# Performance work log

Measured on AMD Instinct MI355X. Metric: run time of the kernel, lower is better.

Reference implementation:

```python
import jax, jax.numpy as jnp
import numpy as np

HEADS = 8


def setup_inputs() -> dict:
    key = jax.random.key(0)
    k1, k2, k3, k4, k5, k6 = jax.random.split(key, 6)
    B, S, E = 2, 2048, 512
    D = E // HEADS
    return {
        "values": jax.random.normal(k1, (B, S, E), dtype=jnp.float32),
        "keys": jax.random.normal(k2, (B, S, E), dtype=jnp.float32),
        "queries": jax.random.normal(k3, (B, S, E), dtype=jnp.float32),
        "mask": jax.random.randint(k4, (B, 1, 1, S), 0, 2, dtype=jnp.int32),
        "W_v": jax.random.normal(k5, (D, D), dtype=jnp.float32) * (1.0 / np.sqrt(D)),
        "W_o": jax.random.normal(k6, (E, E), dtype=jnp.float32) * (1.0 / np.sqrt(E)),
        "b_o": jnp.zeros((E,), dtype=jnp.float32),
    }


def reference(values, keys, queries, mask, W_v, W_o, b_o):
    B, S, E = queries.shape
    H = HEADS
    D = E // H
    # reshape to (b, s, h, d) and apply the SAME W_v linear to v, k, q
    # (faithful to the original, which calls self.values on all three)
    v = jnp.einsum('bshd,ed->bshe', values.reshape(B, -1, H, D), W_v)
    k = jnp.einsum('bshd,ed->bshe', keys.reshape(B, -1, H, D), W_v)
    q = jnp.einsum('bshd,ed->bshe', queries.reshape(B, -1, H, D), W_v)
    # unscaled attention scores (original has no 1/sqrt(d))
    energy = jnp.einsum('bqhd,bkhd->bhqk', q, k)  # (b, h, q, k)
    energy = jnp.where(mask == 0, -jnp.inf, energy)
    attn = jax.nn.softmax(energy, axis=3)
    out = jnp.einsum('bhqk,bkhd->bqhd', attn, v)  # (b, q, h, d)
    out = out.reshape(B, S, E)
    return out @ W_o.T + b_o
```

## Files before the change

kernel.cpp:

```cpp
#include <hip/hip_runtime.h>


#define B_ 2
#define S_ 2048
#define E_ 512
#define H_ 8
#define D_ 64

#define LOG2E 1.4426950408889634f
#define KEEP_BIAS (-92.332483f)

typedef unsigned short ushort_t;
typedef __attribute__((ext_vector_type(8))) short short8;
typedef __attribute__((ext_vector_type(8))) _Float16 half8;
typedef __attribute__((ext_vector_type(4))) float f32x4;

__device__ __forceinline__ ushort_t f2bs(float x) {
    union { float f; unsigned int u; } a; a.f = x;
    unsigned int u = a.u;
    u += 0x7fffu + ((u >> 16) & 1u);
    return (ushort_t)(u >> 16);
}
__device__ __forceinline__ float bs2f(ushort_t h) {
    union { unsigned int u; float f; } a; a.u = ((unsigned int)h) << 16;
    return a.f;
}
__device__ __forceinline__ ushort_t f2hs(float x) {
    _Float16 h = (_Float16)x;
    ushort_t u; __builtin_memcpy(&u, &h, 2);
    return u;
}
__device__ __forceinline__ void split16(const float4* g, ushort_t* hi, ushort_t* lo) {
    #pragma unroll
    for (int q = 0; q < 4; ++q) {
        float4 f = g[q];
        float vv[4] = {f.x, f.y, f.z, f.w};
        #pragma unroll
        for (int j = 0; j < 4; ++j) {
            ushort_t h = f2bs(vv[j]);
            hi[q * 4 + j] = h;
            lo[q * 4 + j] = f2bs(vv[j] - bs2f(h));
        }
    }
}

__global__ void __launch_bounds__(256) proj_mfma(
    const float* __restrict__ quer, const float* __restrict__ keys,
    const float* __restrict__ vals, const float* __restrict__ Wv,
    const float* __restrict__ Wo,
    ushort_t* __restrict__ qf, ushort_t* __restrict__ kf,
    ushort_t* __restrict__ vt, ushort_t* __restrict__ Wob)
{
    __shared__ ushort_t Ah[64 * 72], Al[64 * 72];
    __shared__ ushort_t Bh[64 * 72], Bl[64 * 72];
    const int tens = blockIdx.y;
    const int bx = blockIdx.x;
    const int t = threadIdx.x;

    if (tens == 3) {
        if (bx < 128) {
            int g = (bx * 256 + t) * 8;
            float4 f0 = *(const float4*)(Wo + g);
            float4 f1 = *(const float4*)(Wo + g + 4);
            ushort_t tmp[8] = {f2bs(f0.x), f2bs(f0.y), f2bs(f0.z), f2bs(f0.w),
                               f2bs(f1.x), f2bs(f1.y), f2bs(f1.z), f2bs(f1.w)};
            *(uint4*)&Wob[g] = *(uint4*)tmp;
        }
        return;
    }

    const float* src = tens == 0 ? quer : (tens == 1 ? keys : vals);
    const int st = bx & 31, bh = bx >> 5;
    const int b = bh >> 3, h = bh & 7;
    const int s0 = st * 64;

    {
        int e = t >> 2, dg = (t & 3) * 16;
        ushort_t th[16], tl[16];
        split16((const float4*)(Wv + e * 64 + dg), th, tl);
        *(uint4*)&Bh[e * 72 + dg] = *(uint4*)th;  *(uint4*)&Bh[e * 72 + dg + 8] = *(uint4*)(th + 8);
        *(uint4*)&Bl[e * 72 + dg] = *(uint4*)tl;  *(uint4*)&Bl[e * 72 + dg + 8] = *(uint4*)(tl + 8);
    }
    {
        int row = t >> 2, cg = (t & 3) * 16;
        const float* g = src + ((size_t)b * S_ + s0 + row) * 512 + h * 64 + cg;
        ushort_t th[16], tl[16];
        split16((const float4*)g, th, tl);
        *(uint4*)&Ah[row * 72 + cg] = *(uint4*)th;  *(uint4*)&Ah[row * 72 + cg + 8] = *(uint4*)(th + 8);
        *(uint4*)&Al[row * 72 + cg] = *(uint4*)tl;  *(uint4*)&Al[row * 72 + cg + 8] = *(uint4*)(tl + 8);
    }
    __syncthreads();

    const int w = t >> 6, lm = t & 15, quad = (t >> 4) & 3;
    f32x4 acc[4];
    #pragma unroll
    for (int nt = 0; nt < 4; ++nt) acc[nt] = (f32x4){0.f, 0.f, 0.f, 0.f};

    __builtin_amdgcn_s_setprio(1);
    #pragma unroll
    for (int kk = 0; kk < 2; ++kk) {
        short8 ah = *(const short8*)&Ah[(w * 16 + lm) * 72 + kk * 32 + quad * 8];
        short8 al = *(const short8*)&Al[(w * 16 + lm) * 72 + kk * 32 + quad * 8];
        #pragma unroll
        for (int nt = 0; nt < 4; ++nt) {
            short8 bh8 = *(const short8*)&Bh[(nt * 16 + lm) * 72 + kk * 32 + quad * 8];
            short8 bl8 = *(const short8*)&Bl[(nt * 16 + lm) * 72 + kk * 32 + quad * 8];
            acc[nt] = __builtin_amdgcn_mfma_f32_16x16x32_bf16(ah, bh8, acc[nt], 0, 0, 0);
            acc[nt] = __builtin_amdgcn_mfma_f32_16x16x32_bf16(al, bh8, acc[nt], 0, 0, 0);
            acc[nt] = __builtin_amdgcn_mfma_f32_16x16x32_bf16(ah, bl8, acc[nt], 0, 0, 0);
        }
    }
    __builtin_amdgcn_s_setprio(0);

    if (tens < 2) {
        ushort_t* dst = tens == 0 ? qf : kf;
        const float sc = tens == 0 ? LOG2E : 1.0f;
        #pragma unroll
        for (int nt = 0; nt < 4; ++nt) {
            #pragma unroll
            for (int r = 0; r < 4; ++r) {
                size_t addr = ((size_t)bh * S_ + s0 + w * 16 + quad * 4 + r) * 64 + nt * 16 + lm;
                dst[addr] = f2hs(acc[nt][r] * sc);
            }
        }
    } else {
        #pragma unroll
        for (int nt = 0; nt < 4; ++nt) {
            unsigned int p0 = (unsigned int)f2bs(acc[nt][0]) | ((unsigned int)f2bs(acc[nt][1]) << 16);
            unsigned int p1 = (unsigned int)f2bs(acc[nt][2]) | ((unsigned int)f2bs(acc[nt][3]) << 16);
            uint2 pk; pk.x = p0; pk.y = p1;
            size_t addr = ((size_t)bh * 64 + nt * 16 + lm) * S_ + s0 + w * 16 + quad * 4;
            *(uint2*)&vt[addr] = pk;
        }
    }
}

__global__ void __launch_bounds__(512, 4) attn_mfma(
    const ushort_t* __restrict__ qf, const ushort_t* __restrict__ kf,
    const ushort_t* __restrict__ vt, const int* __restrict__ mask,
    ushort_t* __restrict__ ctx)
{
    __shared__ ushort_t Ks[2][64 * 72];
    __shared__ ushort_t Vt[2][64 * 72];
    __shared__ ushort_t Ps[8 * 16 * 72];
    __shared__ float    mb[2][64];

    const int bx = blockIdx.x;
    const int qt = bx & 31;
    const int bh = bx >> 5;
    const int b  = bh >> 3;
    const int t  = threadIdx.x;
    const int w  = t >> 6;
    const int wq = w & 3;
    const int ws = w >> 2;
    const int lm = t & 15, quad = (t >> 4) & 3;
    const int q0 = qt * 64;
    const int wbase = w * 16 * 72;

    const int srow = t >> 3;
    const int scg  = (t & 7) * 8;
    const size_t kgbase = ((size_t)bh * S_ + srow) * 64 + scg;
    const size_t vgbase = ((size_t)bh * 64 + srow) * S_ + scg;

    half8 aq[2];
    {
        size_t qrow = ((size_t)bh * S_ + q0 + wq * 16 + lm) * 64 + quad * 8;
        aq[0] = *(const half8*)&qf[qrow];
        aq[1] = *(const half8*)&qf[qrow + 32];
    }
    short8 ones;
    #pragma unroll
    for (int j = 0; j < 8; ++j) ones[j] = (short)0x3F80;

    f32x4 acc[4];
    #pragma unroll
    for (int nt = 0; nt < 4; ++nt) acc[nt] = (f32x4){0.f, 0.f, 0.f, 0.f};
    f32x4 acc_l = (f32x4){0.f, 0.f, 0.f, 0.f};

    {
        *(uint4*)&Ks[0][srow * 72 + scg] = *(const uint4*)&kf[kgbase];
        *(uint4*)&Ks[1][srow * 72 + scg] = *(const uint4*)&kf[kgbase + 4096];
        *(uint4*)&Vt[0][srow * 72 + scg] = *(const uint4*)&vt[vgbase];
        *(uint4*)&Vt[1][srow * 72 + scg] = *(const uint4*)&vt[vgbase + 64];
        if (t < 128) mb[t >> 6][t & 63] = mask[b * S_ + t] ? KEEP_BIAS : -1e30f;
    }
    __syncthreads();

    for (int is = 0; is < S_ / 128; ++is) {
        const bool pf = (is + 1) < (S_ / 128);

        uint4 pk0, pk1, pv0, pv1; int mnx = 0;
        if (pf) {
            size_t ko = kgbase + (size_t)(2 * (is + 1)) * 4096;
            pk0 = *(const uint4*)&kf[ko];
            pk1 = *(const uint4*)&kf[ko + 4096];
            size_t vo = vgbase + (size_t)(2 * (is + 1)) * 64;
            pv0 = *(const uint4*)&vt[vo];
            pv1 = *(const uint4*)&vt[vo + 64];
            if (t < 128) mnx = mask[b * S_ + (2 * (is + 1)) * 64 + t];
        }

        const ushort_t* Kc = Ks[ws];
        const ushort_t* Vc = Vt[ws];

        #pragma unroll
        for (int nt = 0; nt < 4; ++nt) {
            f32x4 s = *(const f32x4*)&mb[ws][nt * 16 + quad * 4];
            __builtin_amdgcn_s_setprio(1);
            #pragma unroll
            for (int kk = 0; kk < 2; ++kk) {
                half8 ak = *(const half8*)&Kc[(nt * 16 + lm) * 72 + kk * 32 + quad * 8];
                s = __builtin_amdgcn_mfma_f32_16x16x32_f16(ak, aq[kk], s, 0, 0, 0);
            }
            __builtin_amdgcn_s_setprio(0);
            float p0 = __builtin_amdgcn_exp2f(s[0]);
            float p1 = __builtin_amdgcn_exp2f(s[1]);
            float p2 = __builtin_amdgcn_exp2f(s[2]);
            float p3 = __builtin_amdgcn_exp2f(s[3]);
            uint2 pkd;
            pkd.x = (unsigned int)f2bs(p0) | ((unsigned int)f2bs(p1) << 16);
            pkd.y = (unsigned int)f2bs(p2) | ((unsigned int)f2bs(p3) << 16);
            *(uint2*)&Ps[wbase + lm * 72 + nt * 16 + quad * 4] = pkd;
        }

        __builtin_amdgcn_s_setprio(1);
        #pragma unroll
        for (int kk = 0; kk < 2; ++kk) {
            short8 ap = *(const short8*)&Ps[wbase + lm * 72 + kk * 32 + quad * 8];
            #pragma unroll
            for (int nt = 0; nt < 4; ++nt) {
                short8 bv = *(const short8*)&Vc[(nt * 16 + lm) * 72 + kk * 32 + quad * 8];
                acc[nt] = __builtin_amdgcn_mfma_f32_16x16x32_bf16(ap, bv, acc[nt], 0, 0, 0);
            }
            acc_l = __builtin_amdgcn_mfma_f32_16x16x32_bf16(ap, ones, acc_l, 0, 0, 0);
        }
        __builtin_amdgcn_s_setprio(0);

        __syncthreads();
        if (pf) {
            *(uint4*)&Ks[0][srow * 72 + scg] = pk0;
            *(uint4*)&Ks[1][srow * 72 + scg] = pk1;
            *(uint4*)&Vt[0][srow * 72 + scg] = pv0;
            *(uint4*)&Vt[1][srow * 72 + scg] = pv1;
            if (t < 128) mb[t >> 6][t & 63] = mnx ? KEEP_BIAS : -1e30f;
            __syncthreads();
        }
    }

    float* cf = (float*)Ps;
    const int lane = t & 63;
    __syncthreads();
    if (ws == 1) {
        const int base = (wq * 64 + lane) * 18;
        #pragma unroll
        for (int nt = 0; nt < 4; ++nt) {
            #pragma unroll
            for (int r = 0; r < 4; r += 2) {
                float2 v2; v2.x = acc[nt][r]; v2.y = acc[nt][r + 1];
                *(float2*)&cf[base + nt * 4 + r] = v2;
            }
        }
    }
    __syncthreads();
    if (ws == 0) {
        const int base = (wq * 64 + lane) * 18;
        #pragma unroll
        for (int nt = 0; nt < 4; ++nt) {
            #pragma unroll
            for (int r = 0; r < 4; ++r) acc[nt][r] += cf[base + nt * 4 + r];
        }
    }
    __syncthreads();
    if (ws == 1) {
        const int base = (wq * 64 + lane) * 5;
        #pragma unroll
        for (int r = 0; r < 4; ++r) cf[base + r] = acc_l[r];
    }
    __syncthreads();

    if (ws == 0) {
        const int base = (wq * 64 + lane) * 5;
        #pragma unroll
        for (int r = 0; r < 4; ++r) acc_l[r] += cf[base + r];
        const int h = bh & 7;
        #pragma unroll
        for (int r = 0; r < 4; ++r) {
            float inv = 1.f / acc_l[r];
            int s = q0 + wq * 16 + quad * 4 + r;
            #pragma unroll
            for (int nt = 0; nt < 4; ++nt) {
                int d = nt * 16 + lm;
                ctx[((size_t)b * S_ + s) * E_ + h * D_ + d] = f2bs(acc[nt][r] * inv);
            }
        }
    }
}

__global__ void __launch_bounds__(512, 4) outproj_mfma(
    const ushort_t* __restrict__ ctx, const ushort_t* __restrict__ Wob,
    const float* __restrict__ bo, float* __restrict__ out)
{
    __shared__ ushort_t sm[4][64 * 72];
    const int m0 = blockIdx.x * 64, n0 = blockIdx.y * 64;
    const int t = threadIdx.x;
    const int w = t >> 6, wq = w & 3, wk = w >> 2;
    const int lm = t & 15, quad = (t >> 4) & 3;
    const int srow = t >> 3, scg = (t & 7) * 8;

    const size_t abase = (size_t)(m0 + srow) * E_ + scg;
    const size_t bbase = (size_t)(n0 + srow) * E_ + scg;

    f32x4 acc[4];
    #pragma unroll
    for (int nt = 0; nt < 4; ++nt) acc[nt] = (f32x4){0.f, 0.f, 0.f, 0.f};

    *(uint4*)&sm[0][srow * 72 + scg] = *(const uint4*)&ctx[abase];
    *(uint4*)&sm[1][srow * 72 + scg] = *(const uint4*)&ctx[abase + 256];
    *(uint4*)&sm[2][srow * 72 + scg] = *(const uint4*)&Wob[bbase];
    *(uint4*)&sm[3][srow * 72 + scg] = *(const uint4*)&Wob[bbase + 256];
    __syncthreads();

    const ushort_t* Ac = sm[wk];
    const ushort_t* Bc = sm[2 + wk];

    for (int is = 0; is < 4; ++is) {
        const bool pf = is < 3;
        uint4 pa0, pa1, pb0, pb1;
        if (pf) {
            pa0 = *(const uint4*)&ctx[abase + (size_t)(is + 1) * 64];
            pa1 = *(const uint4*)&ctx[abase + 256 + (size_t)(is + 1) * 64];
            pb0 = *(const uint4*)&Wob[bbase + (size_t)(is + 1) * 64];
            pb1 = *(const uint4*)&Wob[bbase + 256 + (size_t)(is + 1) * 64];
        }

        __builtin_amdgcn_s_setprio(1);
        #pragma unroll
        for (int kk = 0; kk < 2; ++kk) {
            short8 a = *(const short8*)&Ac[(wq * 16 + lm) * 72 + kk * 32 + quad * 8];
            #pragma unroll
            for (int nt = 0; nt < 4; ++nt) {
                short8 bb = *(const short8*)&Bc[(nt * 16 + lm) * 72 + kk * 32 + quad * 8];
                acc[nt] = __builtin_amdgcn_mfma_f32_16x16x32_bf16(a, bb, acc[nt], 0, 0, 0);
            }
        }
        __builtin_amdgcn_s_setprio(0);

        __syncthreads();
        if (pf) {
            *(uint4*)&sm[0][srow * 72 + scg] = pa0;
            *(uint4*)&sm[1][srow * 72 + scg] = pa1;
            *(uint4*)&sm[2][srow * 72 + scg] = pb0;
            *(uint4*)&sm[3][srow * 72 + scg] = pb1;
            __syncthreads();
        }
    }

    float* cf = (float*)sm;
    const int lane = t & 63;
    if (wk == 1) {
        const int base = (wq * 64 + lane) * 18;
        #pragma unroll
        for (int nt = 0; nt < 4; ++nt) {
            #pragma unroll
            for (int r = 0; r < 4; r += 2) {
                float2 v2; v2.x = acc[nt][r]; v2.y = acc[nt][r + 1];
                *(float2*)&cf[base + nt * 4 + r] = v2;
            }
        }
    }
    __syncthreads();
    if (wk == 0) {
        const int base = (wq * 64 + lane) * 18;
        #pragma unroll
        for (int nt = 0; nt < 4; ++nt) {
            float bias = bo[n0 + nt * 16 + lm];
            #pragma unroll
            for (int r = 0; r < 4; ++r) {
                int m = m0 + wq * 16 + quad * 4 + r;
                out[(size_t)m * E_ + n0 + nt * 16 + lm] =
                    acc[nt][r] + cf[base + nt * 4 + r] + bias;
            }
        }
    }
}

extern "C" void kernel_launch(void* const* d_in, const int* in_sizes, int n_in,
                              void* d_out, int out_size, void* d_ws, size_t ws_size,
                              hipStream_t stream) {
    const float* vals = (const float*)d_in[0];
    const float* keys = (const float*)d_in[1];
    const float* quer = (const float*)d_in[2];
    const int*   mask = (const int*)d_in[3];
    const float* Wv   = (const float*)d_in[4];
    const float* Wo   = (const float*)d_in[5];
    const float* bo   = (const float*)d_in[6];
    float* out = (float*)d_out;

    const size_t N = (size_t)B_ * H_ * S_ * D_;
    ushort_t* ws  = (ushort_t*)d_ws;
    ushort_t* qf  = ws;
    ushort_t* kf  = ws + N;
    ushort_t* vt  = ws + 2 * N;
    ushort_t* ctx = ws + 3 * N;
    ushort_t* Wob = ws + 4 * N;

    proj_mfma<<<dim3(B_ * H_ * (S_ / 64), 4), 256, 0, stream>>>(
        quer, keys, vals, Wv, Wo, qf, kf, vt, Wob);
    attn_mfma<<<B_ * H_ * (S_ / 64), 512, 0, stream>>>(qf, kf, vt, mask, ctx);
    outproj_mfma<<<dim3((B_ * S_) / 64, E_ / 64), 512, 0, stream>>>(ctx, Wob, bo, out);
}
```

Baseline: 131.4 us.

## Give each attention wave 32 queries and split keys four ways

Each wave now covers 32 query rows, sharing every loaded K fragment and V fragment across two query groups. Waves are laid out as 2 query groups by 4 key splits with 256-key stages, and each wave stages a whole 64-row K or V tile. The combine becomes a two-level tree reduction through shared memory, and block indices are swizzled to spread heads across CUs. The aim is fewer LDS reads per MFMA and fewer barriers, at the cost of more registers and LDS, reflected in launch bounds lowered to 2 blocks per CU.

```diff
diff --git a/kernel.cpp b/kernel.cpp
--- a/kernel.cpp
+++ b/kernel.cpp
@@ -135,69 +135,77 @@
     }
 }
 
-__global__ void __launch_bounds__(512, 4) attn_mfma(
+__global__ void __launch_bounds__(512, 2) attn_mfma(
     const ushort_t* __restrict__ qf, const ushort_t* __restrict__ kf,
     const ushort_t* __restrict__ vt, const int* __restrict__ mask,
     ushort_t* __restrict__ ctx)
 {
-    __shared__ ushort_t Ks[2][64 * 72];
-    __shared__ ushort_t Vt[2][64 * 72];
-    __shared__ ushort_t Ps[8 * 16 * 72];
-    __shared__ float    mb[2][64];
-
-    const int bx = blockIdx.x;
+    __shared__ ushort_t Ks[4][64 * 72];
+    __shared__ ushort_t Vt[4][64 * 72];
+    __shared__ ushort_t Ps[8][32 * 72];
+    __shared__ float    mb[4][64];
+
+    const int bx0 = blockIdx.x;
+    const int bx = (bx0 & 7) * 64 + (bx0 >> 3);
     const int qt = bx & 31;
     const int bh = bx >> 5;
     const int b  = bh >> 3;
     const int t  = threadIdx.x;
     const int w  = t >> 6;
-    const int wq = w & 3;
-    const int ws = w >> 2;
+    const int wq = w & 1;
+    const int ws = w >> 1;
     const int lm = t & 15, quad = (t >> 4) & 3;
+    const int lane = t & 63;
     const int q0 = qt * 64;
-    const int wbase = w * 16 * 72;
-
-    const int srow = t >> 3;
-    const int scg  = (t & 7) * 8;
-    const size_t kgbase = ((size_t)bh * S_ + srow) * 64 + scg;
-    const size_t vgbase = ((size_t)bh * 64 + srow) * S_ + scg;
-
-    half8 aq[2];
+
+    const int stile = w & 3;
+    const bool isV = w >= 4;
+    const size_t kstage0 = ((size_t)bh * S_ + stile * 64 + lane) * 64;
+    const size_t vstage0 = ((size_t)bh * 64 + lane) * S_ + stile * 64;
+    ushort_t* sdst = isV ? &Vt[stile][lane * 72] : &Ks[stile][lane * 72];
+    const ushort_t* sgl = isV ? vt : kf;
+    const size_t sg0 = isV ? vstage0 : kstage0;
+    const size_t sgstep = isV ? 256 : 16384;
+
+    half8 aq[2][2];
+    #pragma unroll
+    for (int qg = 0; qg < 2; ++qg) {
+        size_t qrow = ((size_t)bh * S_ + q0 + wq * 32 + qg * 16 + lm) * 64 + quad * 8;
+        aq[qg][0] = *(const half8*)&qf[qrow];
+        aq[qg][1] = *(const half8*)&qf[qrow + 32];
+    }
+    short8 ones;
+    #pragma unroll
+    for (int j = 0; j < 8; ++j) ones[j] = (short)0x3F80;
+
+    f32x4 acc[2][4];
+    f32x4 accl[2];
+    #pragma unroll
+    for (int qg = 0; qg < 2; ++qg) {
+        accl[qg] = (f32x4){0.f, 0.f, 0.f, 0.f};
+        #pragma unroll
+        for (int nt = 0; nt < 4; ++nt) acc[qg][nt] = (f32x4){0.f, 0.f, 0.f, 0.f};
+    }
+
     {
-        size_t qrow = ((size_t)bh * S_ + q0 + wq * 16 + lm) * 64 + quad * 8;
-        aq[0] = *(const half8*)&qf[qrow];
-        aq[1] = *(const half8*)&qf[qrow + 32];
-    }
-    short8 ones;
-    #pragma unroll
-    for (int j = 0; j < 8; ++j) ones[j] = (short)0x3F80;
-
-    f32x4 acc[4];
-    #pragma unroll
-    for (int nt = 0; nt < 4; ++nt) acc[nt] = (f32x4){0.f, 0.f, 0.f, 0.f};
-    f32x4 acc_l = (f32x4){0.f, 0.f, 0.f, 0.f};
-
-    {
-        *(uint4*)&Ks[0][srow * 72 + scg] = *(const uint4*)&kf[kgbase];
-        *(uint4*)&Ks[1][srow * 72 + scg] = *(const uint4*)&kf[kgbase + 4096];
-        *(uint4*)&Vt[0][srow * 72 + scg] = *(const uint4*)&vt[vgbase];
-        *(uint4*)&Vt[1][srow * 72 + scg] = *(const uint4*)&vt[vgbase + 64];
-        if (t < 128) mb[t >> 6][t & 63] = mask[b * S_ + t] ? KEEP_BIAS : -1e30f;
-    }
-    __syncthreads();
-
-    for (int is = 0; is < S_ / 128; ++is) {
-        const bool pf = (is + 1) < (S_ / 128);
-
-        uint4 pk0, pk1, pv0, pv1; int mnx = 0;
+        uint4 st[8];
+        #pragma unroll
+        for (int j = 0; j < 8; ++j) st[j] = *(const uint4*)&sgl[sg0 + j * 8];
+        #pragma unroll
+        for (int j = 0; j < 8; ++j) *(uint4*)&sdst[j * 8] = st[j];
+        if (t < 256) mb[t >> 6][t & 63] = mask[b * S_ + t] ? KEEP_BIAS : -1e30f;
+    }
+    __syncthreads();
+
+    for (int is = 0; is < 8; ++is) {
+        const bool pf = is < 7;
+
+        uint4 st[8]; int mnx = 0;
         if (pf) {
-            size_t ko = kgbase + (size_t)(2 * (is + 1)) * 4096;
-            pk0 = *(const uint4*)&kf[ko];
-            pk1 = *(const uint4*)&kf[ko + 4096];
-            size_t vo = vgbase + (size_t)(2 * (is + 1)) * 64;
-            pv0 = *(const uint4*)&vt[vo];
-            pv1 = *(const uint4*)&vt[vo + 64];
-            if (t < 128) mnx = mask[b * S_ + (2 * (is + 1)) * 64 + t];
+            size_t g = sg0 + (size_t)(is + 1) * sgstep;
+            #pragma unroll
+            for (int j = 0; j < 8; ++j) st[j] = *(const uint4*)&sgl[g + j * 8];
+            if (t < 256) mnx = mask[b * S_ + (is + 1) * 256 + t];
         }
 
         const ushort_t* Kc = Ks[ws];
@@ -205,92 +213,117 @@
 
         #pragma unroll
         for (int nt = 0; nt < 4; ++nt) {
-            f32x4 s = *(const f32x4*)&mb[ws][nt * 16 + quad * 4];
+            f32x4 binit = *(const f32x4*)&mb[ws][nt * 16 + quad * 4];
+            f32x4 s0v = binit, s1v = binit;
             __builtin_amdgcn_s_setprio(1);
             #pragma unroll
             for (int kk = 0; kk < 2; ++kk) {
                 half8 ak = *(const half8*)&Kc[(nt * 16 + lm) * 72 + kk * 32 + quad * 8];
-                s = __builtin_amdgcn_mfma_f32_16x16x32_f16(ak, aq[kk], s, 0, 0, 0);
+                s0v = __builtin_amdgcn_mfma_f32_16x16x32_f16(ak, aq[0][kk], s0v, 0, 0, 0);
+                s1v = __builtin_amdgcn_mfma_f32_16x16x32_f16(ak, aq[1][kk], s1v, 0, 0, 0);
             }
             __builtin_amdgcn_s_setprio(0);
-            float p0 = __builtin_amdgcn_exp2f(s[0]);
-            float p1 = __builtin_amdgcn_exp2f(s[1]);
-            float p2 = __builtin_amdgcn_exp2f(s[2]);
-            float p3 = __builtin_amdgcn_exp2f(s[3]);
-            uint2 pkd;
-            pkd.x = (unsigned int)f2bs(p0) | ((unsigned int)f2bs(p1) << 16);
-            pkd.y = (unsigned int)f2bs(p2) | ((unsigned int)f2bs(p3) << 16);
-            *(uint2*)&Ps[wbase + lm * 72 + nt * 16 + quad * 4] = pkd;
+            uint2 p0d, p1d;
+            p0d.x = (unsigned int)f2bs(__builtin_amdgcn_exp2f(s0v[0])) |
+                    ((unsigned int)f2bs(__builtin_amdgcn_exp2f(s0v[1])) << 16);
+            p0d.y = (unsigned int)f2bs(__builtin_amdgcn_exp2f(s0v[2])) |
+                    ((unsigned int)f2bs(__builtin_amdgcn_exp2f(s0v[3])) << 16);
+            p1d.x = (unsigned int)f2bs(__builtin_amdgcn_exp2f(s1v[0])) |
+                    ((unsigned int)f2bs(__builtin_amdgcn_exp2f(s1v[1])) << 16);
+            p1d.y = (unsigned int)f2bs(__builtin_amdgcn_exp2f(s1v[2])) |
+                    ((unsigned int)f2bs(__builtin_amdgcn_exp2f(s1v[3])) << 16);
+            *(uint2*)&Ps[w][(lm) * 72 + nt * 16 + quad * 4]      = p0d;
+            *(uint2*)&Ps[w][(16 + lm) * 72 + nt * 16 + quad * 4] = p1d;
         }
 
         __builtin_amdgcn_s_setprio(1);
         #pragma unroll
         for (int kk = 0; kk < 2; ++kk) {
-            short8 ap = *(const short8*)&Ps[wbase + lm * 72 + kk * 32 + quad * 8];
+            short8 ap0 = *(const short8*)&Ps[w][(lm) * 72 + kk * 32 + quad * 8];
+            short8 ap1 = *(const short8*)&Ps[w][(16 + lm) * 72 + kk * 32 + quad * 8];
             #pragma unroll
             for (int nt = 0; nt < 4; ++nt) {
                 short8 bv = *(const short8*)&Vc[(nt * 16 + lm) * 72 + kk * 32 + quad * 8];
-                acc[nt] = __builtin_amdgcn_mfma_f32_16x16x32_bf16(ap, bv, acc[nt], 0, 0, 0);
-            }
-            acc_l = __builtin_amdgcn_mfma_f32_16x16x32_bf16(ap, ones, acc_l, 0, 0, 0);
+                acc[0][nt] = __builtin_amdgcn_mfma_f32_16x16x32_bf16(ap0, bv, acc[0][nt], 0, 0, 0);
+                acc[1][nt] = __builtin_amdgcn_mfma_f32_16x16x32_bf16(ap1, bv, acc[1][nt], 0, 0, 0);
+            }
+            accl[0] = __builtin_amdgcn_mfma_f32_16x16x32_bf16(ap0, ones, accl[0], 0, 0, 0);
+            accl[1] = __builtin_amdgcn_mfma_f32_16x16x32_bf16(ap1, ones, accl[1], 0, 0, 0);
         }
         __builtin_amdgcn_s_setprio(0);
 
         __syncthreads();
         if (pf) {
-            *(uint4*)&Ks[0][srow * 72 + scg] = pk0;
-            *(uint4*)&Ks[1][srow * 72 + scg] = pk1;
-            *(uint4*)&Vt[0][srow * 72 + scg] = pv0;
-            *(uint4*)&Vt[1][srow * 72 + scg] = pv1;
-            if (t < 128) mb[t >> 6][t & 63] = mnx ? KEEP_BIAS : -1e30f;
+            #pragma unroll
+            for (int j = 0; j < 8; ++j) *(uint4*)&sdst[j * 8] = st[j];
+            if (t < 256) mb[t >> 6][t & 63] = mnx ? KEEP_BIAS : -1e30f;
             __syncthreads();
         }
     }
 
-    float* cf = (float*)Ps;
-    const int lane = t & 63;
-    __syncthreads();
-    if (ws == 1) {
-        const int base = (wq * 64 + lane) * 18;
-        #pragma unroll
-        for (int nt = 0; nt < 4; ++nt) {
-            #pragma unroll
-            for (int r = 0; r < 4; r += 2) {
-                float2 v2; v2.x = acc[nt][r]; v2.y = acc[nt][r + 1];
-                *(float2*)&cf[base + nt * 4 + r] = v2;
-            }
+    float* cfO = (float*)Ks;
+    float* cfL = (float*)Vt;
+    __syncthreads();
+    if (ws & 1) {
+        const int wid = wq * 2 + (ws >> 1);
+        #pragma unroll
+        for (int qg = 0; qg < 2; ++qg) {
+            const int bO = ((wid * 2 + qg) * 64 + lane) * 17;
+            #pragma unroll
+            for (int nt = 0; nt < 4; ++nt)
+                #pragma unroll
+                for (int r = 0; r < 4; ++r) cfO[bO + nt * 4 + r] = acc[qg][nt][r];
+            const int bL = ((wid * 2 + qg) * 64 + lane) * 5;
+            #pragma unroll
+            for (int r = 0; r < 4; ++r) cfL[bL + r] = accl[qg][r];
+        }
+    }
+    __syncthreads();
+    if (!(ws & 1)) {
+        const int wid = wq * 2 + (ws >> 1);
+        #pragma unroll
+        for (int qg = 0; qg < 2; ++qg) {
+            const int bO = ((wid * 2 + qg) * 64 + lane) * 17;
+            #pragma unroll
+            for (int nt = 0; nt < 4; ++nt)
+                #pragma unroll
+                for (int r = 0; r < 4; ++r) acc[qg][nt][r] += cfO[bO + nt * 4 + r];
+            const int bL = ((wid * 2 + qg) * 64 + lane) * 5;
+            #pragma unroll
+            for (int r = 0; r < 4; ++r) accl[qg][r] += cfL[bL + r];
+        }
+    }
+    __syncthreads();
+    if (ws == 2) {
+        #pragma unroll
+        for (int qg = 0; qg < 2; ++qg) {
+            const int bO = ((wq * 2 + qg) * 64 + lane) * 17;
+            #pragma unroll
+            for (int nt = 0; nt < 4; ++nt)
+                #pragma unroll
+                for (int r = 0; r < 4; ++r) cfO[bO + nt * 4 + r] = acc[qg][nt][r];
+            const int bL = ((wq * 2 + qg) * 64 + lane) * 5;
+            #pragma unroll
+            for (int r = 0; r < 4; ++r) cfL[bL + r] = accl[qg][r];
         }
     }
     __syncthreads();
     if (ws == 0) {
-        const int base = (wq * 64 + lane) * 18;
-        #pragma unroll
-        for (int nt = 0; nt < 4; ++nt) {
-            #pragma unroll
-            for (int r = 0; r < 4; ++r) acc[nt][r] += cf[base + nt * 4 + r];
-        }
-    }
-    __syncthreads();
-    if (ws == 1) {
-        const int base = (wq * 64 + lane) * 5;
-        #pragma unroll
-        for (int r = 0; r < 4; ++r) cf[base + r] = acc_l[r];
-    }
-    __syncthreads();
-
-    if (ws == 0) {
-        const int base = (wq * 64 + lane) * 5;
-        #pragma unroll
-        for (int r = 0; r < 4; ++r) acc_l[r] += cf[base + r];
         const int h = bh & 7;
         #pragma unroll
-        for (int r = 0; r < 4; ++r) {
-            float inv = 1.f / acc_l[r];
-            int s = q0 + wq * 16 + quad * 4 + r;
-            #pragma unroll
-            for (int nt = 0; nt < 4; ++nt) {
-                int d = nt * 16 + lm;
-                ctx[((size_t)b * S_ + s) * E_ + h * D_ + d] = f2bs(acc[nt][r] * inv);
+        for (int qg = 0; qg < 2; ++qg) {
+            const int bO = ((wq * 2 + qg) * 64 + lane) * 17;
+            const int bL = ((wq * 2 + qg) * 64 + lane) * 5;
+            #pragma unroll
+            for (int r = 0; r < 4; ++r) {
+                float l = accl[qg][r] + cfL[bL + r];
+                float inv = 1.f / l;
+                int s = q0 + wq * 32 + qg * 16 + quad * 4 + r;
+                #pragma unroll
+                for (int nt = 0; nt < 4; ++nt) {
+                    float o = acc[qg][nt][r] + cfO[bO + nt * 4 + r];
+                    ctx[((size_t)b * S_ + s) * E_ + h * D_ + nt * 16 + lm] = f2bs(o * inv);
+                }
             }
         }
     }
```

After: 192.1 us. 1.46x slower.

## Read K and V straight from global memory in attention, drop LDS staging

Applied to the files above, without the earlier changes.

The attention kernel no longer stages K and V tiles through double-buffered shared memory with block-wide barriers. Each wave now loads its MFMA operands directly from global memory (relying on L2/L1), and each wave-half walks its own half of the key range with no per-iteration syncs. The mask bias for the whole sequence is precomputed into LDS once, blocks are remapped so neighbouring blocks share a head for cache locality, and the cross-half reduction is merged into fewer barriers. The cost is more global/L1 traffic and exposed load latency, since direct loads are less coalesced and nothing is explicitly prefetched.

```diff
diff --git a/kernel.cpp b/kernel.cpp
--- a/kernel.cpp
+++ b/kernel.cpp
@@ -140,12 +140,11 @@
     const ushort_t* __restrict__ vt, const int* __restrict__ mask,
     ushort_t* __restrict__ ctx)
 {
-    __shared__ ushort_t Ks[2][64 * 72];
-    __shared__ ushort_t Vt[2][64 * 72];
-    __shared__ ushort_t Ps[8 * 16 * 72];
-    __shared__ float    mb[2][64];
-
-    const int bx = blockIdx.x;
+    __shared__ ushort_t Ps[8][16 * 72];
+    __shared__ float    biasL[S_];
+
+    const int bx0 = blockIdx.x;
+    const int bx = (bx0 & 7) * 64 + (bx0 >> 3);
     const int qt = bx & 31;
     const int bh = bx >> 5;
     const int b  = bh >> 3;
@@ -154,143 +153,99 @@
     const int wq = w & 3;
     const int ws = w >> 2;
     const int lm = t & 15, quad = (t >> 4) & 3;
+    const int lane = t & 63;
     const int q0 = qt * 64;
-    const int wbase = w * 16 * 72;
-
-    const int srow = t >> 3;
-    const int scg  = (t & 7) * 8;
-    const size_t kgbase = ((size_t)bh * S_ + srow) * 64 + scg;
-    const size_t vgbase = ((size_t)bh * 64 + srow) * S_ + scg;
-
-    half8 aq[2];
+
+    {
+        int4 m4 = *(const int4*)&mask[b * S_ + t * 4];
+        float4 bv;
+        bv.x = m4.x ? KEEP_BIAS : -1e30f;
+        bv.y = m4.y ? KEEP_BIAS : -1e30f;
+        bv.z = m4.z ? KEEP_BIAS : -1e30f;
+        bv.w = m4.w ? KEEP_BIAS : -1e30f;
+        *(float4*)&biasL[t * 4] = bv;
+    }
+
+    half8 aq0, aq1;
     {
         size_t qrow = ((size_t)bh * S_ + q0 + wq * 16 + lm) * 64 + quad * 8;
-        aq[0] = *(const half8*)&qf[qrow];
-        aq[1] = *(const half8*)&qf[qrow + 32];
+        aq0 = *(const half8*)&qf[qrow];
+        aq1 = *(const half8*)&qf[qrow + 32];
     }
     short8 ones;
     #pragma unroll
     for (int j = 0; j < 8; ++j) ones[j] = (short)0x3F80;
 
+    const ushort_t* kB = kf + ((size_t)bh * S_ + lm) * 64 + quad * 8;
+    const ushort_t* vB = vt + ((size_t)bh * 64 + lm) * S_ + quad * 8;
+
     f32x4 acc[4];
+    f32x4 accl = (f32x4){0.f, 0.f, 0.f, 0.f};
     #pragma unroll
     for (int nt = 0; nt < 4; ++nt) acc[nt] = (f32x4){0.f, 0.f, 0.f, 0.f};
-    f32x4 acc_l = (f32x4){0.f, 0.f, 0.f, 0.f};
-
-    {
-        *(uint4*)&Ks[0][srow * 72 + scg] = *(const uint4*)&kf[kgbase];
-        *(uint4*)&Ks[1][srow * 72 + scg] = *(const uint4*)&kf[kgbase + 4096];
-        *(uint4*)&Vt[0][srow * 72 + scg] = *(const uint4*)&vt[vgbase];
-        *(uint4*)&Vt[1][srow * 72 + scg] = *(const uint4*)&vt[vgbase + 64];
-        if (t < 128) mb[t >> 6][t & 63] = mask[b * S_ + t] ? KEEP_BIAS : -1e30f;
-    }
-    __syncthreads();
-
-    for (int is = 0; is < S_ / 128; ++is) {
-        const bool pf = (is + 1) < (S_ / 128);
-
-        uint4 pk0, pk1, pv0, pv1; int mnx = 0;
-        if (pf) {
-            size_t ko = kgbase + (size_t)(2 * (is + 1)) * 4096;
-            pk0 = *(const uint4*)&kf[ko];
-            pk1 = *(const uint4*)&kf[ko + 4096];
-            size_t vo = vgbase + (size_t)(2 * (is + 1)) * 64;
-            pv0 = *(const uint4*)&vt[vo];
-            pv1 = *(const uint4*)&vt[vo + 64];
-            if (t < 128) mnx = mask[b * S_ + (2 * (is + 1)) * 64 + t];
-        }
-
-        const ushort_t* Kc = Ks[ws];
-        const ushort_t* Vc = Vt[ws];
-
-        #pragma unroll
-        for (int nt = 0; nt < 4; ++nt) {
-            f32x4 s = *(const f32x4*)&mb[ws][nt * 16 + quad * 4];
+
+    __syncthreads();
+
+    for (int kc = ws * 16; kc < ws * 16 + 16; ++kc) {
+        #pragma unroll
+        for (int nt = 0; nt < 4; ++nt) {
+            const ushort_t* ka = kB + (size_t)(kc * 64 + nt * 16) * 64;
+            half8 ak0 = *(const half8*)&ka[0];
+            half8 ak1 = *(const half8*)&ka[32];
+            f32x4 s = *(const f32x4*)&biasL[kc * 64 + nt * 16 + quad * 4];
             __builtin_amdgcn_s_setprio(1);
-            #pragma unroll
-            for (int kk = 0; kk < 2; ++kk) {
-                half8 ak = *(const half8*)&Kc[(nt * 16 + lm) * 72 + kk * 32 + quad * 8];
-                s = __builtin_amdgcn_mfma_f32_16x16x32_f16(ak, aq[kk], s, 0, 0, 0);
-            }
+            s = __builtin_amdgcn_mfma_f32_16x16x32_f16(ak0, aq0, s, 0, 0, 0);
+            s = __builtin_amdgcn_mfma_f32_16x16x32_f16(ak1, aq1, s, 0, 0, 0);
             __builtin_amdgcn_s_setprio(0);
-            float p0 = __builtin_amdgcn_exp2f(s[0]);
-            float p1 = __builtin_amdgcn_exp2f(s[1]);
-            float p2 = __builtin_amdgcn_exp2f(s[2]);
-            float p3 = __builtin_amdgcn_exp2f(s[3]);
             uint2 pkd;
-            pkd.x = (unsigned int)f2bs(p0) | ((unsigned int)f2bs(p1) << 16);
-            pkd.y = (unsigned int)f2bs(p2) | ((unsigned int)f2bs(p3) << 16);
-            *(uint2*)&Ps[wbase + lm * 72 + nt * 16 + quad * 4] = pkd;
+            pkd.x = (unsigned int)f2bs(__builtin_amdgcn_exp2f(s[0])) |
+                    ((unsigned int)f2bs(__builtin_amdgcn_exp2f(s[1])) << 16);
+            pkd.y = (unsigned int)f2bs(__builtin_amdgcn_exp2f(s[2])) |
+                    ((unsigned int)f2bs(__builtin_amdgcn_exp2f(s[3])) << 16);
+            *(uint2*)&Ps[w][lm * 72 + nt * 16 + quad * 4] = pkd;
         }
 
         __builtin_amdgcn_s_setprio(1);
         #pragma unroll
         for (int kk = 0; kk < 2; ++kk) {
-            short8 ap = *(const short8*)&Ps[wbase + lm * 72 + kk * 32 + quad * 8];
+            short8 ap = *(const short8*)&Ps[w][lm * 72 + kk * 32 + quad * 8];
             #pragma unroll
             for (int nt = 0; nt < 4; ++nt) {
-                short8 bv = *(const short8*)&Vc[(nt * 16 + lm) * 72 + kk * 32 + quad * 8];
+                short8 bv = *(const short8*)&vB[(size_t)(nt * 16) * S_ + kc * 64 + kk * 32];
                 acc[nt] = __builtin_amdgcn_mfma_f32_16x16x32_bf16(ap, bv, acc[nt], 0, 0, 0);
             }
-            acc_l = __builtin_amdgcn_mfma_f32_16x16x32_bf16(ap, ones, acc_l, 0, 0, 0);
+            accl = __builtin_amdgcn_mfma_f32_16x16x32_bf16(ap, ones, accl, 0, 0, 0);
         }
         __builtin_amdgcn_s_setprio(0);
-
-        __syncthreads();
-        if (pf) {
-            *(uint4*)&Ks[0][srow * 72 + scg] = pk0;
-            *(uint4*)&Ks[1][srow * 72 + scg] = pk1;
-            *(uint4*)&Vt[0][srow * 72 + scg] = pv0;
-            *(uint4*)&Vt[1][srow * 72 + scg] = pv1;
-            if (t < 128) mb[t >> 6][t & 63] = mnx ? KEEP_BIAS : -1e30f;
-            __syncthreads();
-        }
-    }
-
-    float* cf = (float*)Ps;
-    const int lane = t & 63;
+    }
+
+    float* cfO = (float*)Ps;
+    float* cfL = biasL;
     __syncthreads();
     if (ws == 1) {
-        const int base = (wq * 64 + lane) * 18;
-        #pragma unroll
-        for (int nt = 0; nt < 4; ++nt) {
-            #pragma unroll
-            for (int r = 0; r < 4; r += 2) {
-                float2 v2; v2.x = acc[nt][r]; v2.y = acc[nt][r + 1];
-                *(float2*)&cf[base + nt * 4 + r] = v2;
-            }
-        }
+        const int bO = (wq * 64 + lane) * 17;
+        const int bL = (wq * 64 + lane) * 5;
+        #pragma unroll
+        for (int nt = 0; nt < 4; ++nt)
+            #pragma unroll
+            for (int r = 0; r < 4; ++r) cfO[bO + nt * 4 + r] = acc[nt][r];
+        #pragma unroll
+        for (int r = 0; r < 4; ++r) cfL[bL + r] = accl[r];
     }
     __syncthreads();
     if (ws == 0) {
-        const int base = (wq * 64 + lane) * 18;
-        #pragma unroll
-        for (int nt = 0; nt < 4; ++nt) {
-            #pragma unroll
-            for (int r = 0; r < 4; ++r) acc[nt][r] += cf[base + nt * 4 + r];
-        }
-    }
-    __syncthreads();
-    if (ws == 1) {
-        const int base = (wq * 64 + lane) * 5;
-        #pragma unroll
-        for (int r = 0; r < 4; ++r) cf[base + r] = acc_l[r];
-    }
-    __syncthreads();
-
-    if (ws == 0) {
-        const int base = (wq * 64 + lane) * 5;
-        #pragma unroll
-        for (int r = 0; r < 4; ++r) acc_l[r] += cf[base + r];
+        const int bO = (wq * 64 + lane) * 17;
+        const int bL = (wq * 64 + lane) * 5;
         const int h = bh & 7;
         #pragma unroll
         for (int r = 0; r < 4; ++r) {
-            float inv = 1.f / acc_l[r];
+            float l = accl[r] + cfL[bL + r];
+            float inv = 1.f / l;
             int s = q0 + wq * 16 + quad * 4 + r;
             #pragma unroll
             for (int nt = 0; nt < 4; ++nt) {
-                int d = nt * 16 + lm;
-                ctx[((size_t)b * S_ + s) * E_ + h * D_ + d] = f2bs(acc[nt][r] * inv);
+                float o = acc[nt][r] + cfO[bO + nt * 4 + r];
+                ctx[((size_t)b * S_ + s) * E_ + h * D_ + nt * 16 + lm] = f2bs(o * inv);
             }
         }
     }
```

Result: slower. 206.4 us (+57.1%).
